# Optimization experiments

Hardware: AMD Instinct MI355X
Metric: run time of the kernel (lower is better)

Reference implementation:

```python
import jax, jax.numpy as jnp
import numpy as np


def _lstm(x, h0, c0, Wih, Whh, b):
    """Single-layer LSTM, batch_first input x: [B,T,D]. PyTorch gate order i,f,g,o.
    Returns (h_seq [T,B,H], h_T [B,H], c_T [B,H])."""
    xs = jnp.swapaxes(x, 0, 1)  # [T,B,D]

    def step(carry, xt):
        h, c = carry
        gates = xt @ Wih.T + h @ Whh.T + b  # [B,4H]
        i, f, g, o = jnp.split(gates, 4, axis=-1)
        c = jax.nn.sigmoid(f) * c + jax.nn.sigmoid(i) * jnp.tanh(g)
        h = jax.nn.sigmoid(o) * jnp.tanh(c)
        return (h, c), h

    (h, c), hs = jax.lax.scan(step, (h0, c0), xs)
    return hs, h, c


def setup_inputs() -> dict:
    key = jax.random.key(0)
    ks = jax.random.split(key, 16)
    B, T, Tf, Tu = 256, 365, 15, 76
    Dh, Df, Du, H = 64, 32, 16, 256
    s = 1.0 / np.sqrt(H)  # torch-style uniform scale, approximated with scaled normals
    return {
        "x_d": jax.random.normal(ks[0], (B, T, Dh), jnp.float32),
        "x_f": jax.random.normal(ks[1], (B, Tf, Df), jnp.float32),
        "x_ff": jax.random.normal(ks[2], (B, Tu, Du), jnp.float32),
        "enc_Wih": jax.random.normal(ks[3], (4 * H, Dh), jnp.float32) * s,
        "enc_Whh": jax.random.normal(ks[4], (4 * H, H), jnp.float32) * s,
        "enc_b": jax.random.normal(ks[5], (4 * H,), jnp.float32) * s,
        "decf_Wih": jax.random.normal(ks[6], (4 * H, Df), jnp.float32) * s,
        "decf_Whh": jax.random.normal(ks[7], (4 * H, H), jnp.float32) * s,
        "decf_b": jax.random.normal(ks[8], (4 * H,), jnp.float32) * s,
        "decu_Wih": jax.random.normal(ks[9], (4 * H, Du), jnp.float32) * s,
        "decu_Whh": jax.random.normal(ks[10], (4 * H, H), jnp.float32) * s,
        "decu_b": jax.random.normal(ks[11], (4 * H,), jnp.float32) * s,
        "head_W": jax.random.normal(ks[12], (1, H), jnp.float32) * s,
        "head_b": jax.random.normal(ks[13], (1,), jnp.float32) * s,
    }


def reference(x_d, x_f, x_ff, enc_Wih, enc_Whh, enc_b,
              decf_Wih, decf_Whh, decf_b, decu_Wih, decu_Whh, decu_b,
              head_W, head_b):
    B = x_d.shape[0]
    H = enc_Whh.shape[1]
    Tf = x_f.shape[1]
    Tu = x_ff.shape[1]
    horizon = Tf + Tu
    h0 = jnp.zeros((B, H), x_d.dtype)
    c0 = jnp.zeros((B, H), x_d.dtype)

    # Encoder over historical sequence
    _, h, c = _lstm(x_d, h0, c0, enc_Wih, enc_Whh, enc_b)

    # Forecast decoder: one LSTM step per horizon step + linear head (dropout = eval identity)
    hs_f, h, c = _lstm(x_f, h, c, decf_Wih, decf_Whh, decf_b)  # [Tf,B,H]
    out_f = (jnp.einsum('tbh,oh->tbo', hs_f, head_W)[..., 0] + head_b[0]).T  # [B,Tf]

    # Future decoder, continuing the hidden state
    hs_u, h, c = _lstm(x_ff, h, c, decu_Wih, decu_Whh, decu_b)  # [Tu,B,H]
    out_u = (jnp.einsum('tbh,oh->tbo', hs_u, head_W)[..., 0] + head_b[0]).T  # [B,Tu]

    # Faithful to original: both loops write outputs[:, t], so the future loop
    # overwrites the first Tu columns.
    outputs = jnp.zeros((B, horizon), x_d.dtype)
    outputs = outputs.at[:, :Tf].set(out_f)
    outputs = outputs.at[:, :Tu].set(out_u)
    return outputs
```

## Files before the change

kernel.cpp:

```cpp
#include <hip/hip_runtime.h>
#include <stdint.h>


typedef __attribute__((ext_vector_type(8))) short short8;
typedef __attribute__((ext_vector_type(4))) float f32x4;
typedef __attribute__((ext_vector_type(2))) unsigned int u32x2;

#define L2E 1.4426950408889634f

__device__ __forceinline__ uint16_t f2bf(float f) {
  uint32_t x = __float_as_uint(f);
  x += 0x7fffu + ((x >> 16) & 1u);
  return (uint16_t)(x >> 16);
}
__device__ __forceinline__ uint32_t pk2(float a, float b) {
  return (uint32_t)f2bf(a) | ((uint32_t)f2bf(b) << 16);
}
__device__ __forceinline__ uint32_t cvtpk(float lo, float hi) {
  uint32_t r;
  asm("v_cvt_pk_bf16_f32 %0, %1, %2" : "=v"(r) : "v"(lo), "v"(hi));
  return r;
}
__device__ __forceinline__ float bfhalf(uint32_t w, int hi) {
  return __uint_as_float(hi ? (w & 0xffff0000u) : (w << 16));
}
__device__ __forceinline__ f32x4 MFMA(short8 a, short8 b, f32x4 c) {
  return __builtin_amdgcn_mfma_f32_16x16x32_bf16(a, b, c, 0, 0, 0);
}
__device__ __forceinline__ float ex2(float x) { return __builtin_amdgcn_exp2f(x); }
__device__ __forceinline__ float rcp(float x) { return __builtin_amdgcn_rcpf(x); }

__device__ __forceinline__ void lgkm_barrier() {
  __builtin_amdgcn_sched_barrier(0);
  asm volatile("s_waitcnt lgkmcnt(0)" ::: "memory");
  __builtin_amdgcn_s_barrier();
  __builtin_amdgcn_sched_barrier(0);
}

__global__ void init_kernel(float* c_state, uint16_t* h_state, float* out) {
  int i = blockIdx.x * 256 + threadIdx.x;
  if (i < 65536) { c_state[i] = 0.f; h_state[i] = 0; }
  if (i < 256 * 91) out[i] = 0.f;
}

template <int DIN>
__global__ __launch_bounds__(512) void xproj_kernel(
    const float* __restrict__ x, const float* __restrict__ Wih,
    const float* __restrict__ bias, uint32_t* __restrict__ xp,
    int t0, int T) {
  const int tid = threadIdx.x, w = tid >> 6, l = tid & 63;
  const int l16 = l & 15, lg = l >> 4;
  const int tc = blockIdx.x >> 1;
  const int sub = blockIdx.x & 1;
  const int t = t0 + tc;
  constexpr int KT = (DIN + 31) / 32;

  short8 bfr[8][KT];
  float4 bias4[8];
#pragma unroll
  for (int ni = 0; ni < 8; ++ni) {
    const int n = (w * 8 + ni) * 16 + l16;
    bias4[ni] = *(const float4*)&bias[(w * 8 + ni) * 16 + lg * 4];
#pragma unroll
    for (int kt = 0; kt < KT; ++kt) {
      const int k0 = kt * 32 + lg * 8;
      short8 fr;
#pragma unroll
      for (int e = 0; e < 8; ++e) fr[e] = 0;
      if (k0 + 8 <= DIN) {
        const float* s = Wih + (size_t)n * DIN + k0;
#pragma unroll
        for (int e = 0; e < 8; ++e) fr[e] = (short)f2bf(s[e]);
      }
      bfr[ni][kt] = fr;
    }
  }

  for (int mi = 0; mi < 8; ++mi) {
    const int btile = sub * 8 + mi;
    const int b = btile * 16 + l16;
    short8 af[KT];
#pragma unroll
    for (int kt = 0; kt < KT; ++kt) {
      const int k0 = kt * 32 + lg * 8;
      short8 fr;
#pragma unroll
      for (int e = 0; e < 8; ++e) fr[e] = 0;
      if (k0 + 8 <= DIN) {
        const float* s = x + ((size_t)b * T + t) * DIN + k0;
#pragma unroll
        for (int e = 0; e < 8; ++e) fr[e] = (short)f2bf(s[e]);
      }
      af[kt] = fr;
    }
#pragma unroll
    for (int ni = 0; ni < 8; ++ni) {
      f32x4 acc = {0.f, 0.f, 0.f, 0.f};
#pragma unroll
      for (int kt = 0; kt < KT; ++kt) acc = MFMA(bfr[ni][kt], af[kt], acc);
      const int nt = w * 8 + ni;
      const float sc = ((nt >> 4) == 2) ? (2.f * L2E) : -L2E;
      size_t idx = ((((size_t)tc * 16 + btile) * 64 + nt) * 64 + l) * 2;
      u32x2 v;
      v[0] = pk2((acc[0] + bias4[ni].x) * sc, (acc[1] + bias4[ni].y) * sc);
      v[1] = pk2((acc[2] + bias4[ni].z) * sc, (acc[3] + bias4[ni].w) * sc);
      *(u32x2*)(xp + idx) = v;
    }
  }
}

template <int DO_HEAD>
__global__ __launch_bounds__(512, 2) void rec_kernel(
    const uint32_t* __restrict__ xp, const float* __restrict__ Whh,
    float* __restrict__ c_state, uint16_t* __restrict__ h_state,
    float* __restrict__ out, const float* __restrict__ headW,
    const float* __restrict__ headb, int ct, int tcol0) {
  __shared__ short8 B_lds[8 * 16 * 64];
  __shared__ uint16_t h_lds[2][16][264];
  __shared__ float headbuf[2][16][8];

  const int tid = threadIdx.x, w = tid >> 6, l = tid & 63;
  const int l16 = l & 15, lg = l >> 4;
  const int blk = blockIdx.x, b0 = blk * 16;

  short8 bv[48];
#pragma unroll
  for (int g = 0; g < 4; ++g) {
    const float wsc = (g == 2) ? (2.f * L2E) : -L2E;
#pragma unroll
    for (int nt = 0; nt < 2; ++nt)
#pragma unroll
      for (int kt = 0; kt < 8; ++kt) {
        const int row = (g * 16 + w * 2 + nt) * 16 + l16;
        const float* s = Whh + (size_t)row * 256 + kt * 32 + lg * 8;
        short8 fr;
#pragma unroll
        for (int e = 0; e < 8; ++e) fr[e] = (short)f2bf(s[e] * wsc);
        const int tile = g * 2 + nt;
        if (kt <= 5) bv[tile * 6 + kt] = fr;
        else B_lds[(w * 16 + (kt - 6) * 8 + tile) * 64 + l] = fr;
      }
  }

  float c_reg[2][4];
#pragma unroll
  for (int nt = 0; nt < 2; ++nt) {
    float4 c4 = *(const float4*)&c_state[(size_t)(b0 + l16) * 256 +
                                         (w * 2 + nt) * 16 + lg * 4];
    c_reg[nt][0] = c4.x; c_reg[nt][1] = c4.y;
    c_reg[nt][2] = c4.z; c_reg[nt][3] = c4.w;
  }
  for (int idx = tid; idx < 16 * 256; idx += 512)
    h_lds[0][idx >> 8][idx & 255] = h_state[(size_t)(b0 + (idx >> 8)) * 256 + (idx & 255)];
  float4 hw4[2];
#pragma unroll
  for (int nt = 0; nt < 2; ++nt)
    hw4[nt] = *(const float4*)&headW[(w * 2 + nt) * 16 + lg * 4];
  const float hb = headb[0];

  const uint32_t* xpb = xp + ((size_t)(blk * 64 + w * 2) * 64 + l) * 2;
  u32x2 xpf[2][4];
#pragma unroll
  for (int nt = 0; nt < 2; ++nt)
#pragma unroll
    for (int g = 0; g < 4; ++g)
      xpf[nt][g] = *(const u32x2*)(xpb + (size_t)g * 2048 + nt * 128);

  __syncthreads();

  for (int t = 0; t < ct; ++t) {
    const int cur = t & 1, nxt = cur ^ 1;
    const int tn = (t + 1 < ct) ? t + 1 : t;
    float hp = 0.f;

#pragma unroll
    for (int nt = 0; nt < 2; ++nt) {
      f32x4 acc[4];
#pragma unroll
      for (int g = 0; g < 4; ++g) {
        f32x4 ai;
        ai[0] = bfhalf(xpf[nt][g][0], 0);
        ai[1] = bfhalf(xpf[nt][g][0], 1);
        ai[2] = bfhalf(xpf[nt][g][1], 0);
        ai[3] = bfhalf(xpf[nt][g][1], 1);
        acc[g] = ai;
      }
#pragma unroll
      for (int kt = 0; kt <= 5; ++kt) {
        short8 hf = *(const short8*)(&h_lds[cur][l16][kt * 32 + lg * 8]);
#pragma unroll
        for (int g = 0; g < 4; ++g)
          acc[g] = MFMA(bv[(g * 2 + nt) * 6 + kt], hf, acc[g]);
      }
#pragma unroll
      for (int kt = 6; kt <= 7; ++kt) {
        short8 hf = *(const short8*)(&h_lds[cur][l16][kt * 32 + lg * 8]);
#pragma unroll
        for (int g = 0; g < 4; ++g)
          acc[g] = MFMA(B_lds[(w * 16 + (kt - 6) * 8 + g * 2 + nt) * 64 + l], hf, acc[g]);
      }

      float hv[4];
#pragma unroll
      for (int j = 0; j < 4; ++j) {
        float ei = ex2(acc[0][j]);
        float ef = ex2(acc[1][j]);
        float eg = ex2(acc[2][j]);
        float eo = ex2(acc[3][j]);
        float eip = 1.f + ei, egp = eg + 1.f, efp = 1.f + ef;
        float d1 = eip * egp;
        float R = rcp(d1 * efp);
        float sitg = (eg - 1.f) * efp * R;
        float cc = fmaf(c_reg[nt][j] * d1, R, sitg);
        c_reg[nt][j] = cc;
        float ec = ex2(cc * (2.f * L2E));
        float hh = (ec - 1.f) * rcp((1.f + eo) * (ec + 1.f));
        hv[j] = hh;
      }
      if (DO_HEAD) {
        hp = fmaf(hv[0], hw4[nt].x, hp); hp = fmaf(hv[1], hw4[nt].y, hp);
        hp = fmaf(hv[2], hw4[nt].z, hp); hp = fmaf(hv[3], hw4[nt].w, hp);
      }
      {
        u32x2 hwrd;
        hwrd[0] = cvtpk(hv[0], hv[1]);
        hwrd[1] = cvtpk(hv[2], hv[3]);
        *(u32x2*)(&h_lds[nxt][l16][(w * 2 + nt) * 16 + lg * 4]) = hwrd;
      }
#pragma unroll
      for (int g = 0; g < 4; ++g)
        xpf[nt][g] = *(const u32x2*)(xpb + (size_t)tn * 131072 + g * 2048 + nt * 128);
    }

    if (DO_HEAD) {
      float s = hp;
      s += __shfl_xor(s, 16);
      s += __shfl_xor(s, 32);
      if (lg == 0) headbuf[t & 1][l16][w] = s;
    }

    lgkm_barrier();

    if (DO_HEAD) {
      if (tid < 16) {
        const float* hbp = headbuf[t & 1][tid];
        float s = hbp[0] + hbp[1] + hbp[2] + hbp[3] + hbp[4] + hbp[5] + hbp[6] + hbp[7];
        out[(size_t)(b0 + tid) * 91 + (tcol0 + t)] = s + hb;
      }
    }
  }

#pragma unroll
  for (int nt = 0; nt < 2; ++nt) {
    float4 c4 = {c_reg[nt][0], c_reg[nt][1], c_reg[nt][2], c_reg[nt][3]};
    *(float4*)&c_state[(size_t)(b0 + l16) * 256 + (w * 2 + nt) * 16 + lg * 4] = c4;
  }
  for (int idx = tid; idx < 16 * 256; idx += 512)
    h_state[(size_t)(b0 + (idx >> 8)) * 256 + (idx & 255)] = h_lds[ct & 1][idx >> 8][idx & 255];
}

extern "C" void kernel_launch(void* const* d_in, const int* in_sizes, int n_in,
                              void* d_out, int out_size, void* d_ws, size_t ws_size,
                              hipStream_t stream) {
  const float* headW = (const float*)d_in[12];
  const float* headb = (const float*)d_in[13];
  float* out = (float*)d_out;

  char* ws = (char*)d_ws;
  float* c_state = (float*)ws;
  uint16_t* h_state = (uint16_t*)(ws + 262144);
  uint32_t* xp = (uint32_t*)(ws + 393216);

  int ct_max = 1;
  if (ws_size > 393216 + 512 * 1024) {
    size_t c = (ws_size - 393216) / (512 * 1024);
    ct_max = (c > 365) ? 365 : (int)c;
  }

  init_kernel<<<256, 256, 0, stream>>>(c_state, h_state, out);

  struct Phase { const float* x; const float* Wih; const float* Whh; const float* b; int T; int D; int head; };
  Phase ph[3] = {
      {(const float*)d_in[0], (const float*)d_in[3], (const float*)d_in[4], (const float*)d_in[5],
       in_sizes[0] / (256 * 64), 64, 0},
      {(const float*)d_in[1], (const float*)d_in[6], (const float*)d_in[7], (const float*)d_in[8],
       in_sizes[1] / (256 * 32), 32, 0},
      {(const float*)d_in[2], (const float*)d_in[9], (const float*)d_in[10], (const float*)d_in[11],
       in_sizes[2] / (256 * 16), 16, 1},
  };

  for (int pi = 0; pi < 3; ++pi) {
    const Phase& P = ph[pi];
    for (int t0 = 0; t0 < P.T; t0 += ct_max) {
      int ct = (P.T - t0 < ct_max) ? (P.T - t0) : ct_max;
      dim3 g(ct * 2);
      if (P.D == 64)
        xproj_kernel<64><<<g, 512, 0, stream>>>(P.x, P.Wih, P.b, xp, t0, P.T);
      else if (P.D == 32)
        xproj_kernel<32><<<g, 512, 0, stream>>>(P.x, P.Wih, P.b, xp, t0, P.T);
      else
        xproj_kernel<16><<<g, 512, 0, stream>>>(P.x, P.Wih, P.b, xp, t0, P.T);
      if (P.head)
        rec_kernel<1><<<16, 512, 0, stream>>>(xp, P.Whh, c_state, h_state, out,
                                              headW, headb, ct, t0);
      else
        rec_kernel<0><<<16, 512, 0, stream>>>(xp, P.Whh, c_state, h_state, out,
                                              headW, headb, ct, t0);
    }
  }
}
```

Before: 1.264 ms.

## Split each batch tile's recurrence across two blocks with flag-based h exchange

The recurrent kernel now runs 32 blocks instead of 16. Each pair of blocks shares one 16-row batch tile and each block computes half of the hidden units, so it holds half the Whh fragments and needs half the MFMAs per step. After every step each block writes its half of h (and its partial head sum) to global memory with agent-scope atomic stores, bumps a flag, and spins on its partner's flag before loading the other half into LDS. This uses more CUs to shorten the serial per-step latency, at the cost of a cross-block global-memory handshake on every timestep. It also relies on both blocks of a pair being co-resident and on ordering through relaxed atomics plus vmcnt waits.

```diff
diff --git a/kernel.cpp b/kernel.cpp
--- a/kernel.cpp
+++ b/kernel.cpp
@@ -36,11 +36,18 @@
   __builtin_amdgcn_s_barrier();
   __builtin_amdgcn_sched_barrier(0);
 }
-
-__global__ void init_kernel(float* c_state, uint16_t* h_state, float* out) {
+__device__ __forceinline__ void vm_drain4() {
+  __builtin_amdgcn_sched_barrier(0);
+  asm volatile("s_waitcnt vmcnt(4)" ::: "memory");
+  __builtin_amdgcn_sched_barrier(0);
+}
+
+__global__ void init_kernel(float* c_state, uint16_t* h_state, float* out,
+                            uint32_t* flags) {
   int i = blockIdx.x * 256 + threadIdx.x;
   if (i < 65536) { c_state[i] = 0.f; h_state[i] = 0; }
   if (i < 256 * 91) out[i] = 0.f;
+  if (i < 96) flags[i] = 0;
 }
 
 template <int DIN>
@@ -114,149 +121,180 @@
     const uint32_t* __restrict__ xp, const float* __restrict__ Whh,
     float* __restrict__ c_state, uint16_t* __restrict__ h_state,
     float* __restrict__ out, const float* __restrict__ headW,
-    const float* __restrict__ headb, int ct, int tcol0) {
-  __shared__ short8 B_lds[8 * 16 * 64];
+    const float* __restrict__ headb, uint32_t* __restrict__ flags,
+    unsigned long long* __restrict__ hx, uint32_t* __restrict__ hxh,
+    int ct, int t0, int phase) {
+  __shared__ short8 B_lds[64 * 64];
   __shared__ uint16_t h_lds[2][16][264];
-  __shared__ float headbuf[2][16][8];
+  __shared__ float headbuf[16][8];
 
   const int tid = threadIdx.x, w = tid >> 6, l = tid & 63;
   const int l16 = l & 15, lg = l >> 4;
-  const int blk = blockIdx.x, b0 = blk * 16;
-
-  short8 bv[48];
+  const int blk = blockIdx.x;
+  const int pair = blk & 15, s = blk >> 4, sp = 1 - s;
+  const int b0 = pair * 16;
+  const int ctile = s * 8 + w;
+  uint32_t* const pflag = flags + (phase * 16 + pair) * 2 + sp;
+  uint32_t* const myflag = flags + (phase * 16 + pair) * 2 + s;
+
+  short8 bv[24];
 #pragma unroll
   for (int g = 0; g < 4; ++g) {
     const float wsc = (g == 2) ? (2.f * L2E) : -L2E;
 #pragma unroll
-    for (int nt = 0; nt < 2; ++nt)
-#pragma unroll
-      for (int kt = 0; kt < 8; ++kt) {
-        const int row = (g * 16 + w * 2 + nt) * 16 + l16;
-        const float* s = Whh + (size_t)row * 256 + kt * 32 + lg * 8;
-        short8 fr;
-#pragma unroll
-        for (int e = 0; e < 8; ++e) fr[e] = (short)f2bf(s[e] * wsc);
-        const int tile = g * 2 + nt;
-        if (kt <= 5) bv[tile * 6 + kt] = fr;
-        else B_lds[(w * 16 + (kt - 6) * 8 + tile) * 64 + l] = fr;
-      }
-  }
-
-  float c_reg[2][4];
-#pragma unroll
-  for (int nt = 0; nt < 2; ++nt) {
+    for (int kt = 0; kt < 8; ++kt) {
+      const int row = (g * 16 + ctile) * 16 + l16;
+      const float* sw = Whh + (size_t)row * 256 + kt * 32 + lg * 8;
+      short8 fr;
+#pragma unroll
+      for (int e = 0; e < 8; ++e) fr[e] = (short)f2bf(sw[e] * wsc);
+      if (kt <= 5) bv[g * 6 + kt] = fr;
+      else B_lds[(w * 8 + g * 2 + (kt - 6)) * 64 + l] = fr;
+    }
+  }
+
+  float c_reg[4];
+  {
     float4 c4 = *(const float4*)&c_state[(size_t)(b0 + l16) * 256 +
-                                         (w * 2 + nt) * 16 + lg * 4];
-    c_reg[nt][0] = c4.x; c_reg[nt][1] = c4.y;
-    c_reg[nt][2] = c4.z; c_reg[nt][3] = c4.w;
+                                         ctile * 16 + lg * 4];
+    c_reg[0] = c4.x; c_reg[1] = c4.y; c_reg[2] = c4.z; c_reg[3] = c4.w;
   }
   for (int idx = tid; idx < 16 * 256; idx += 512)
     h_lds[0][idx >> 8][idx & 255] = h_state[(size_t)(b0 + (idx >> 8)) * 256 + (idx & 255)];
-  float4 hw4[2];
-#pragma unroll
-  for (int nt = 0; nt < 2; ++nt)
-    hw4[nt] = *(const float4*)&headW[(w * 2 + nt) * 16 + lg * 4];
+  float4 hw4 = *(const float4*)&headW[ctile * 16 + lg * 4];
   const float hb = headb[0];
 
-  const uint32_t* xpb = xp + ((size_t)(blk * 64 + w * 2) * 64 + l) * 2;
-  u32x2 xpf[2][4];
-#pragma unroll
-  for (int nt = 0; nt < 2; ++nt)
-#pragma unroll
-    for (int g = 0; g < 4; ++g)
-      xpf[nt][g] = *(const u32x2*)(xpb + (size_t)g * 2048 + nt * 128);
+  const uint32_t* xpb = xp + ((size_t)(pair * 64 + ctile) * 64 + l) * 2;
+  u32x2 xpf[4];
+#pragma unroll
+  for (int g = 0; g < 4; ++g)
+    xpf[g] = *(const u32x2*)(xpb + (size_t)g * 2048);
 
   __syncthreads();
 
   for (int t = 0; t < ct; ++t) {
     const int cur = t & 1, nxt = cur ^ 1;
     const int tn = (t + 1 < ct) ? t + 1 : t;
-    float hp = 0.f;
-
-#pragma unroll
-    for (int nt = 0; nt < 2; ++nt) {
-      f32x4 acc[4];
+    const int par = t & 1;
+    const uint32_t tgt = (uint32_t)(t0 + t + 1);
+    float hsum = 0.f;
+
+    f32x4 acc[4];
+#pragma unroll
+    for (int g = 0; g < 4; ++g) {
+      f32x4 ai;
+      ai[0] = bfhalf(xpf[g][0], 0);
+      ai[1] = bfhalf(xpf[g][0], 1);
+      ai[2] = bfhalf(xpf[g][1], 0);
+      ai[3] = bfhalf(xpf[g][1], 1);
+      acc[g] = ai;
+    }
+#pragma unroll
+    for (int kt = 0; kt < 8; ++kt) {
+      short8 hf = *(const short8*)(&h_lds[cur][l16][kt * 32 + lg * 8]);
 #pragma unroll
       for (int g = 0; g < 4; ++g) {
-        f32x4 ai;
-        ai[0] = bfhalf(xpf[nt][g][0], 0);
-        ai[1] = bfhalf(xpf[nt][g][0], 1);
-        ai[2] = bfhalf(xpf[nt][g][1], 0);
-        ai[3] = bfhalf(xpf[nt][g][1], 1);
-        acc[g] = ai;
-      }
-#pragma unroll
-      for (int kt = 0; kt <= 5; ++kt) {
-        short8 hf = *(const short8*)(&h_lds[cur][l16][kt * 32 + lg * 8]);
-#pragma unroll
-        for (int g = 0; g < 4; ++g)
-          acc[g] = MFMA(bv[(g * 2 + nt) * 6 + kt], hf, acc[g]);
-      }
-#pragma unroll
-      for (int kt = 6; kt <= 7; ++kt) {
-        short8 hf = *(const short8*)(&h_lds[cur][l16][kt * 32 + lg * 8]);
-#pragma unroll
-        for (int g = 0; g < 4; ++g)
-          acc[g] = MFMA(B_lds[(w * 16 + (kt - 6) * 8 + g * 2 + nt) * 64 + l], hf, acc[g]);
-      }
-
-      float hv[4];
-#pragma unroll
-      for (int j = 0; j < 4; ++j) {
-        float ei = ex2(acc[0][j]);
-        float ef = ex2(acc[1][j]);
-        float eg = ex2(acc[2][j]);
-        float eo = ex2(acc[3][j]);
-        float eip = 1.f + ei, egp = eg + 1.f, efp = 1.f + ef;
-        float d1 = eip * egp;
-        float R = rcp(d1 * efp);
-        float sitg = (eg - 1.f) * efp * R;
-        float cc = fmaf(c_reg[nt][j] * d1, R, sitg);
-        c_reg[nt][j] = cc;
-        float ec = ex2(cc * (2.f * L2E));
-        float hh = (ec - 1.f) * rcp((1.f + eo) * (ec + 1.f));
-        hv[j] = hh;
-      }
-      if (DO_HEAD) {
-        hp = fmaf(hv[0], hw4[nt].x, hp); hp = fmaf(hv[1], hw4[nt].y, hp);
-        hp = fmaf(hv[2], hw4[nt].z, hp); hp = fmaf(hv[3], hw4[nt].w, hp);
-      }
-      {
-        u32x2 hwrd;
-        hwrd[0] = cvtpk(hv[0], hv[1]);
-        hwrd[1] = cvtpk(hv[2], hv[3]);
-        *(u32x2*)(&h_lds[nxt][l16][(w * 2 + nt) * 16 + lg * 4]) = hwrd;
-      }
-#pragma unroll
-      for (int g = 0; g < 4; ++g)
-        xpf[nt][g] = *(const u32x2*)(xpb + (size_t)tn * 131072 + g * 2048 + nt * 128);
-    }
+        if (kt <= 5) acc[g] = MFMA(bv[g * 6 + kt], hf, acc[g]);
+        else acc[g] = MFMA(B_lds[(w * 8 + g * 2 + (kt - 6)) * 64 + l], hf, acc[g]);
+      }
+    }
+
+    float hv[4];
+#pragma unroll
+    for (int j = 0; j < 4; ++j) {
+      float ei = ex2(acc[0][j]);
+      float ef = ex2(acc[1][j]);
+      float eg = ex2(acc[2][j]);
+      float eo = ex2(acc[3][j]);
+      float eip = 1.f + ei, egp = eg + 1.f, efp = 1.f + ef;
+      float d1 = eip * egp;
+      float R = rcp(d1 * efp);
+      float sitg = (eg - 1.f) * efp * R;
+      float cc = fmaf(c_reg[j] * d1, R, sitg);
+      c_reg[j] = cc;
+      float ec = ex2(cc * (2.f * L2E));
+      float hh = (ec - 1.f) * rcp((1.f + eo) * (ec + 1.f));
+      hv[j] = hh;
+    }
+
+    u32x2 hwrd;
+    hwrd[0] = cvtpk(hv[0], hv[1]);
+    hwrd[1] = cvtpk(hv[2], hv[3]);
+    *(u32x2*)(&h_lds[nxt][l16][ctile * 16 + lg * 4]) = hwrd;
+    {
+      unsigned long long v64 =
+          ((unsigned long long)hwrd[1] << 32) | (unsigned long long)hwrd[0];
+      unsigned long long* dst =
+          hx + ((size_t)((pair * 2 + s) * 2 + par) * 512) + (w * 4 + lg) * 16 + l16;
+      __hip_atomic_store(dst, v64, __ATOMIC_RELAXED, __HIP_MEMORY_SCOPE_AGENT);
+    }
+
+#pragma unroll
+    for (int g = 0; g < 4; ++g)
+      xpf[g] = *(const u32x2*)(xpb + (size_t)tn * 131072 + g * 2048);
 
     if (DO_HEAD) {
-      float s = hp;
-      s += __shfl_xor(s, 16);
-      s += __shfl_xor(s, 32);
-      if (lg == 0) headbuf[t & 1][l16][w] = s;
-    }
-
+      float hp = fmaf(hv[0], hw4.x, fmaf(hv[1], hw4.y,
+                 fmaf(hv[2], hw4.z, hv[3] * hw4.w)));
+      hp += __shfl_xor(hp, 16);
+      hp += __shfl_xor(hp, 32);
+      if (lg == 0) headbuf[l16][w] = hp;
+    }
+
+    vm_drain4();
     lgkm_barrier();
 
     if (DO_HEAD) {
       if (tid < 16) {
-        const float* hbp = headbuf[t & 1][tid];
-        float s = hbp[0] + hbp[1] + hbp[2] + hbp[3] + hbp[4] + hbp[5] + hbp[6] + hbp[7];
-        out[(size_t)(b0 + tid) * 91 + (tcol0 + t)] = s + hb;
-      }
-    }
-  }
-
-#pragma unroll
-  for (int nt = 0; nt < 2; ++nt) {
-    float4 c4 = {c_reg[nt][0], c_reg[nt][1], c_reg[nt][2], c_reg[nt][3]};
-    *(float4*)&c_state[(size_t)(b0 + l16) * 256 + (w * 2 + nt) * 16 + lg * 4] = c4;
-  }
-  for (int idx = tid; idx < 16 * 256; idx += 512)
-    h_state[(size_t)(b0 + (idx >> 8)) * 256 + (idx & 255)] = h_lds[ct & 1][idx >> 8][idx & 255];
+        const float* hbp = headbuf[tid];
+        hsum = hbp[0] + hbp[1] + hbp[2] + hbp[3] +
+               hbp[4] + hbp[5] + hbp[6] + hbp[7];
+        __hip_atomic_store(hxh + ((pair * 2 + s) * 2 + par) * 16 + tid,
+                           __float_as_uint(hsum), __ATOMIC_RELAXED,
+                           __HIP_MEMORY_SCOPE_AGENT);
+      }
+      vm_drain4();
+    }
+    if (tid == 0)
+      __hip_atomic_store(myflag, tgt, __ATOMIC_RELAXED, __HIP_MEMORY_SCOPE_AGENT);
+
+    __builtin_amdgcn_sched_barrier(0);
+    uint32_t f;
+    do {
+      f = __hip_atomic_load(pflag, __ATOMIC_RELAXED, __HIP_MEMORY_SCOPE_AGENT);
+    } while ((int)(f - tgt) < 0);
+    __builtin_amdgcn_sched_barrier(0);
+
+    {
+      const unsigned long long* src =
+          hx + ((size_t)((pair * 2 + sp) * 2 + par) * 512) + (w * 4 + lg) * 16 + l16;
+      unsigned long long pv =
+          __hip_atomic_load(src, __ATOMIC_RELAXED, __HIP_MEMORY_SCOPE_AGENT);
+      u32x2 pw;
+      pw[0] = (uint32_t)pv;
+      pw[1] = (uint32_t)(pv >> 32);
+      *(u32x2*)(&h_lds[nxt][l16][sp * 128 + w * 16 + lg * 4]) = pw;
+    }
+    if (DO_HEAD && s == 0) {
+      if (tid < 16) {
+        uint32_t pp = __hip_atomic_load(
+            hxh + ((pair * 2 + sp) * 2 + par) * 16 + tid,
+            __ATOMIC_RELAXED, __HIP_MEMORY_SCOPE_AGENT);
+        out[(size_t)(b0 + tid) * 91 + (t0 + t)] = hsum + __uint_as_float(pp) + hb;
+      }
+    }
+
+    lgkm_barrier();
+  }
+
+  {
+    float4 c4 = {c_reg[0], c_reg[1], c_reg[2], c_reg[3]};
+    *(float4*)&c_state[(size_t)(b0 + l16) * 256 + ctile * 16 + lg * 4] = c4;
+  }
+  if (s == 0)
+    for (int idx = tid; idx < 16 * 256; idx += 512)
+      h_state[(size_t)(b0 + (idx >> 8)) * 256 + (idx & 255)] =
+          h_lds[ct & 1][idx >> 8][idx & 255];
 }
 
 extern "C" void kernel_launch(void* const* d_in, const int* in_sizes, int n_in,
@@ -269,15 +307,18 @@
   char* ws = (char*)d_ws;
   float* c_state = (float*)ws;
   uint16_t* h_state = (uint16_t*)(ws + 262144);
-  uint32_t* xp = (uint32_t*)(ws + 393216);
+  uint32_t* flags = (uint32_t*)(ws + 393216);
+  unsigned long long* hx = (unsigned long long*)(ws + 397312);
+  uint32_t* hxh = (uint32_t*)(ws + 659456);
+  uint32_t* xp = (uint32_t*)(ws + 667648);
 
   int ct_max = 1;
-  if (ws_size > 393216 + 512 * 1024) {
-    size_t c = (ws_size - 393216) / (512 * 1024);
+  if (ws_size > 667648 + 512 * 1024) {
+    size_t c = (ws_size - 667648) / (512 * 1024);
     ct_max = (c > 365) ? 365 : (int)c;
   }
 
-  init_kernel<<<256, 256, 0, stream>>>(c_state, h_state, out);
+  init_kernel<<<256, 256, 0, stream>>>(c_state, h_state, out, flags);
 
   struct Phase { const float* x; const float* Wih; const float* Whh; const float* b; int T; int D; int head; };
   Phase ph[3] = {
@@ -301,11 +342,13 @@
       else
         xproj_kernel<16><<<g, 512, 0, stream>>>(P.x, P.Wih, P.b, xp, t0, P.T);
       if (P.head)
-        rec_kernel<1><<<16, 512, 0, stream>>>(xp, P.Whh, c_state, h_state, out,
-                                              headW, headb, ct, t0);
+        rec_kernel<1><<<32, 512, 0, stream>>>(xp, P.Whh, c_state, h_state, out,
+                                              headW, headb, flags, hx, hxh,
+                                              ct, t0, pi);
       else
-        rec_kernel<0><<<16, 512, 0, stream>>>(xp, P.Whh, c_state, h_state, out,
-                                              headW, headb, ct, t0);
-    }
-  }
-}
+        rec_kernel<0><<<32, 512, 0, stream>>>(xp, P.Whh, c_state, h_state, out,
+                                              headW, headb, flags, hx, hxh,
+                                              ct, t0, pi);
+    }
+  }
+}
```

New measurement: 1.298 ms. +2.7%, slower.

## Fuse encoder and both decoder recurrences into one persistent kernel

Applied to the files above, without the earlier changes.

When the workspace can hold the input projections for all three LSTM phases, the code precomputes them up front and runs a single recurrence kernel that loops over encoder, forecast decoder and future decoder. The cell and hidden state stay in registers and LDS across phases instead of being written to and read back from global memory between launches. Weight and input packing now uses vectorised float4 loads and the hardware bf16 convert instruction in place of scalar rounding. The cost is a larger workspace footprint and Whh reloads inside the fused kernel; the older chunked path is kept as a fallback.

```diff
diff --git a/kernel.cpp b/kernel.cpp
--- a/kernel.cpp
+++ b/kernel.cpp
@@ -5,6 +5,7 @@
 typedef __attribute__((ext_vector_type(8))) short short8;
 typedef __attribute__((ext_vector_type(4))) float f32x4;
 typedef __attribute__((ext_vector_type(2))) unsigned int u32x2;
+typedef __attribute__((ext_vector_type(4))) unsigned int u32x4;
 
 #define L2E 1.4426950408889634f
 
@@ -13,9 +14,6 @@
   x += 0x7fffu + ((x >> 16) & 1u);
   return (uint16_t)(x >> 16);
 }
-__device__ __forceinline__ uint32_t pk2(float a, float b) {
-  return (uint32_t)f2bf(a) | ((uint32_t)f2bf(b) << 16);
-}
 __device__ __forceinline__ uint32_t cvtpk(float lo, float hi) {
   uint32_t r;
   asm("v_cvt_pk_bf16_f32 %0, %1, %2" : "=v"(r) : "v"(lo), "v"(hi));
@@ -29,6 +27,16 @@
 }
 __device__ __forceinline__ float ex2(float x) { return __builtin_amdgcn_exp2f(x); }
 __device__ __forceinline__ float rcp(float x) { return __builtin_amdgcn_rcpf(x); }
+
+__device__ __forceinline__ short8 pack8s(const float* s, float sc) {
+  float4 q0 = *(const float4*)s, q1 = *(const float4*)(s + 4);
+  u32x4 t;
+  t[0] = cvtpk(q0.x * sc, q0.y * sc);
+  t[1] = cvtpk(q0.z * sc, q0.w * sc);
+  t[2] = cvtpk(q1.x * sc, q1.y * sc);
+  t[3] = cvtpk(q1.z * sc, q1.w * sc);
+  return *(short8*)&t;
+}
 
 __device__ __forceinline__ void lgkm_barrier() {
   __builtin_amdgcn_sched_barrier(0);
@@ -67,11 +75,7 @@
       short8 fr;
 #pragma unroll
       for (int e = 0; e < 8; ++e) fr[e] = 0;
-      if (k0 + 8 <= DIN) {
-        const float* s = Wih + (size_t)n * DIN + k0;
-#pragma unroll
-        for (int e = 0; e < 8; ++e) fr[e] = (short)f2bf(s[e]);
-      }
+      if (k0 + 8 <= DIN) fr = pack8s(Wih + (size_t)n * DIN + k0, 1.f);
       bfr[ni][kt] = fr;
     }
   }
@@ -86,11 +90,7 @@
       short8 fr;
 #pragma unroll
       for (int e = 0; e < 8; ++e) fr[e] = 0;
-      if (k0 + 8 <= DIN) {
-        const float* s = x + ((size_t)b * T + t) * DIN + k0;
-#pragma unroll
-        for (int e = 0; e < 8; ++e) fr[e] = (short)f2bf(s[e]);
-      }
+      if (k0 + 8 <= DIN) fr = pack8s(x + ((size_t)b * T + t) * DIN + k0, 1.f);
       af[kt] = fr;
     }
 #pragma unroll
@@ -102,9 +102,154 @@
       const float sc = ((nt >> 4) == 2) ? (2.f * L2E) : -L2E;
       size_t idx = ((((size_t)tc * 16 + btile) * 64 + nt) * 64 + l) * 2;
       u32x2 v;
-      v[0] = pk2((acc[0] + bias4[ni].x) * sc, (acc[1] + bias4[ni].y) * sc);
-      v[1] = pk2((acc[2] + bias4[ni].z) * sc, (acc[3] + bias4[ni].w) * sc);
+      v[0] = cvtpk((acc[0] + bias4[ni].x) * sc, (acc[1] + bias4[ni].y) * sc);
+      v[1] = cvtpk((acc[2] + bias4[ni].z) * sc, (acc[3] + bias4[ni].w) * sc);
       *(u32x2*)(xp + idx) = v;
+    }
+  }
+}
+
+__global__ __launch_bounds__(512, 2) void rec_fused(
+    const uint32_t* __restrict__ xp0, const uint32_t* __restrict__ xp1,
+    const uint32_t* __restrict__ xp2, const float* __restrict__ Whh0,
+    const float* __restrict__ Whh1, const float* __restrict__ Whh2,
+    float* __restrict__ out, const float* __restrict__ headW,
+    const float* __restrict__ headb, int T0, int T1, int T2) {
+  __shared__ short8 B_lds[8 * 16 * 64];
+  __shared__ uint16_t h_lds[2][16][264];
+  __shared__ float headbuf[2][16][8];
+
+  const int tid = threadIdx.x, w = tid >> 6, l = tid & 63;
+  const int l16 = l & 15, lg = l >> 4;
+  const int blk = blockIdx.x, b0 = blk * 16;
+
+  float c_reg[2][4];
+#pragma unroll
+  for (int nt = 0; nt < 2; ++nt)
+#pragma unroll
+    for (int j = 0; j < 4; ++j) c_reg[nt][j] = 0.f;
+  for (int idx = tid; idx < 16 * 264; idx += 512)
+    ((uint16_t*)h_lds)[idx] = 0;
+  float4 hw4[2];
+#pragma unroll
+  for (int nt = 0; nt < 2; ++nt)
+    hw4[nt] = *(const float4*)&headW[(w * 2 + nt) * 16 + lg * 4];
+  const float hb = headb[0];
+
+  int cur = 0;
+  for (int p = 0; p < 3; ++p) {
+    const float* Whh = (p == 0) ? Whh0 : (p == 1) ? Whh1 : Whh2;
+    const uint32_t* xp = (p == 0) ? xp0 : (p == 1) ? xp1 : xp2;
+    const int ct = (p == 0) ? T0 : (p == 1) ? T1 : T2;
+    const bool headf = (p == 2);
+
+    short8 bv[48];
+#pragma unroll
+    for (int g = 0; g < 4; ++g) {
+      const float wsc = (g == 2) ? (2.f * L2E) : -L2E;
+#pragma unroll
+      for (int nt = 0; nt < 2; ++nt)
+#pragma unroll
+        for (int kt = 0; kt < 8; ++kt) {
+          const int row = (g * 16 + w * 2 + nt) * 16 + l16;
+          short8 fr = pack8s(Whh + (size_t)row * 256 + kt * 32 + lg * 8, wsc);
+          const int tile = g * 2 + nt;
+          if (kt <= 5) bv[tile * 6 + kt] = fr;
+          else B_lds[(w * 16 + (kt - 6) * 8 + tile) * 64 + l] = fr;
+        }
+    }
+
+    const uint32_t* xpb = xp + ((size_t)(blk * 64 + w * 2) * 64 + l) * 2;
+    u32x2 xpf[2][4];
+#pragma unroll
+    for (int nt = 0; nt < 2; ++nt)
+#pragma unroll
+      for (int g = 0; g < 4; ++g)
+        xpf[nt][g] = *(const u32x2*)(xpb + (size_t)g * 2048 + nt * 128);
+
+    __syncthreads();
+
+    for (int t = 0; t < ct; ++t) {
+      const int nxt = cur ^ 1;
+      const int tn = (t + 1 < ct) ? t + 1 : t;
+      float hp = 0.f;
+
+#pragma unroll
+      for (int nt = 0; nt < 2; ++nt) {
+        f32x4 acc[4];
+#pragma unroll
+        for (int g = 0; g < 4; ++g) {
+          f32x4 ai;
+          ai[0] = bfhalf(xpf[nt][g][0], 0);
+          ai[1] = bfhalf(xpf[nt][g][0], 1);
+          ai[2] = bfhalf(xpf[nt][g][1], 0);
+          ai[3] = bfhalf(xpf[nt][g][1], 1);
+          acc[g] = ai;
+        }
+#pragma unroll
+        for (int kt = 0; kt <= 5; ++kt) {
+          short8 hf = *(const short8*)(&h_lds[cur][l16][kt * 32 + lg * 8]);
+#pragma unroll
+          for (int g = 0; g < 4; ++g)
+            acc[g] = MFMA(bv[(g * 2 + nt) * 6 + kt], hf, acc[g]);
+        }
+#pragma unroll
+        for (int kt = 6; kt <= 7; ++kt) {
+          short8 hf = *(const short8*)(&h_lds[cur][l16][kt * 32 + lg * 8]);
+#pragma unroll
+          for (int g = 0; g < 4; ++g)
+            acc[g] = MFMA(B_lds[(w * 16 + (kt - 6) * 8 + g * 2 + nt) * 64 + l], hf, acc[g]);
+        }
+
+        float hv[4];
+#pragma unroll
+        for (int j = 0; j < 4; ++j) {
+          float ei = ex2(acc[0][j]);
+          float ef = ex2(acc[1][j]);
+          float eg = ex2(acc[2][j]);
+          float eo = ex2(acc[3][j]);
+          float eip = 1.f + ei, egp = eg + 1.f, efp = 1.f + ef;
+          float d1 = eip * egp;
+          float R = rcp(d1 * efp);
+          float sitg = (eg - 1.f) * efp * R;
+          float cc = fmaf(c_reg[nt][j] * d1, R, sitg);
+          c_reg[nt][j] = cc;
+          float ec = ex2(cc * (2.f * L2E));
+          float hh = (ec - 1.f) * rcp((1.f + eo) * (ec + 1.f));
+          hv[j] = hh;
+        }
+        if (headf) {
+          hp = fmaf(hv[0], hw4[nt].x, hp); hp = fmaf(hv[1], hw4[nt].y, hp);
+          hp = fmaf(hv[2], hw4[nt].z, hp); hp = fmaf(hv[3], hw4[nt].w, hp);
+        }
+        {
+          u32x2 hwrd;
+          hwrd[0] = cvtpk(hv[0], hv[1]);
+          hwrd[1] = cvtpk(hv[2], hv[3]);
+          *(u32x2*)(&h_lds[nxt][l16][(w * 2 + nt) * 16 + lg * 4]) = hwrd;
+        }
+#pragma unroll
+        for (int g = 0; g < 4; ++g)
+          xpf[nt][g] = *(const u32x2*)(xpb + (size_t)tn * 131072 + g * 2048 + nt * 128);
+      }
+
+      if (headf) {
+        float s = hp;
+        s += __shfl_xor(s, 16);
+        s += __shfl_xor(s, 32);
+        if (lg == 0) headbuf[t & 1][l16][w] = s;
+      }
+
+      lgkm_barrier();
+
+      if (headf) {
+        if (tid < 16) {
+          const float* hbp = headbuf[t & 1][tid];
+          float s = hbp[0] + hbp[1] + hbp[2] + hbp[3] + hbp[4] + hbp[5] + hbp[6] + hbp[7];
+          out[(size_t)(b0 + tid) * 91 + t] = s + hb;
+        }
+      }
+      cur = nxt;
     }
   }
 }
@@ -265,8 +410,30 @@
   const float* headW = (const float*)d_in[12];
   const float* headb = (const float*)d_in[13];
   float* out = (float*)d_out;
-
   char* ws = (char*)d_ws;
+
+  const int T0 = in_sizes[0] / (256 * 64);
+  const int T1 = in_sizes[1] / (256 * 32);
+  const int T2 = in_sizes[2] / (256 * 16);
+  const size_t s0 = (size_t)T0 << 19, s1 = (size_t)T1 << 19, s2 = (size_t)T2 << 19;
+
+  if (ws_size >= s0 + s1 + s2) {
+    uint32_t* xp0 = (uint32_t*)ws;
+    uint32_t* xp1 = (uint32_t*)(ws + s0);
+    uint32_t* xp2 = (uint32_t*)(ws + s0 + s1);
+    init_kernel<<<256, 256, 0, stream>>>((float*)ws, (uint16_t*)(ws + 262144), out);
+    xproj_kernel<64><<<dim3(T0 * 2), 512, 0, stream>>>(
+        (const float*)d_in[0], (const float*)d_in[3], (const float*)d_in[5], xp0, 0, T0);
+    xproj_kernel<32><<<dim3(T1 * 2), 512, 0, stream>>>(
+        (const float*)d_in[1], (const float*)d_in[6], (const float*)d_in[8], xp1, 0, T1);
+    xproj_kernel<16><<<dim3(T2 * 2), 512, 0, stream>>>(
+        (const float*)d_in[2], (const float*)d_in[9], (const float*)d_in[11], xp2, 0, T2);
+    rec_fused<<<16, 512, 0, stream>>>(
+        xp0, xp1, xp2, (const float*)d_in[4], (const float*)d_in[7],
+        (const float*)d_in[10], out, headW, headb, T0, T1, T2);
+    return;
+  }
+
   float* c_state = (float*)ws;
   uint16_t* h_state = (uint16_t*)(ws + 262144);
   uint32_t* xp = (uint32_t*)(ws + 393216);
@@ -281,12 +448,9 @@
 
   struct Phase { const float* x; const float* Wih; const float* Whh; const float* b; int T; int D; int head; };
   Phase ph[3] = {
-      {(const float*)d_in[0], (const float*)d_in[3], (const float*)d_in[4], (const float*)d_in[5],
-       in_sizes[0] / (256 * 64), 64, 0},
-      {(const float*)d_in[1], (const float*)d_in[6], (const float*)d_in[7], (const float*)d_in[8],
-       in_sizes[1] / (256 * 32), 32, 0},
-      {(const float*)d_in[2], (const float*)d_in[9], (const float*)d_in[10], (const float*)d_in[11],
-       in_sizes[2] / (256 * 16), 16, 1},
+      {(const float*)d_in[0], (const float*)d_in[3], (const float*)d_in[4], (const float*)d_in[5], T0, 64, 0},
+      {(const float*)d_in[1], (const float*)d_in[6], (const float*)d_in[7], (const float*)d_in[8], T1, 32, 0},
+      {(const float*)d_in[2], (const float*)d_in[9], (const float*)d_in[10], (const float*)d_in[11], T2, 16, 1},
   };
 
   for (int pi = 0; pi < 3; ++pi) {
```

Result: slower. 1.346 ms (+6.4%).
